# Performance work log

Measured on AMD Instinct MI355X. Metric: run time of the kernel, lower is better.

## Reference

```python
import jax, jax.numpy as jnp
import numpy as np

# config (matches init_kwargs)
WZ, WH, WW = 2, 6, 12            # window_size
Z, H, W = 8, 96, 120             # input_shape after patch embedding
DIM, HEADS = 192, 6
DH = DIM // HEADS
SCALE = DH ** 0.5
NZ, NH, NW = Z // WZ, H // WH, W // WW
NWIN = NZ * NH * NW              # 640 windows (B=1)
TW = NZ * NH                     # type_of_windows = 64
ZHW = WZ * WH * WW               # 144 tokens per window
TABLE = (2 * WW - 1) * WH ** 2 * WZ ** 2  # 3312 bias rows


def _pos_index():
    """Earth-specific relative position index, identical to _construct_index."""
    zi = np.arange(WZ); zj = -np.arange(WZ) * WZ
    hi = np.arange(WH); hj = -np.arange(WH) * WH
    w = np.arange(WW)
    c1 = np.stack(np.meshgrid(zi, hi, w, indexing='ij')).reshape(3, -1)
    c2 = np.stack(np.meshgrid(zj, hj, w, indexing='ij')).reshape(3, -1)
    c = (c1[:, :, None] - c2[:, None, :]).transpose(1, 2, 0)  # (N, N, 3)
    c[..., 2] += WW - 1
    c[..., 1] *= 2 * WW - 1
    c[..., 0] *= (2 * WW - 1) * WH ** 2
    return jnp.asarray(c.sum(-1).reshape(-1), dtype=jnp.int32)  # (ZHW*ZHW,)


def setup_inputs() -> dict:
    key = jax.random.key(0)
    ks = jax.random.split(key, 6)
    x = jax.random.normal(ks[0], (NWIN, ZHW, DIM), jnp.float32)
    # shifted-window style additive mask: 0 or -100
    mask = jnp.where(jax.random.uniform(ks[1], (NWIN, ZHW, ZHW)) < 0.1,
                     jnp.float32(-100.0), jnp.float32(0.0))
    w1 = jax.random.normal(ks[2], (DIM, 3 * DIM), jnp.float32) * 0.02
    b1 = jnp.zeros((3 * DIM,), jnp.float32)
    w2 = jax.random.normal(ks[3], (DIM, DIM), jnp.float32) * 0.02
    b2 = jnp.zeros((DIM,), jnp.float32)
    bias_table = jax.random.normal(ks[4], (TABLE, TW, HEADS), jnp.float32) * 0.02
    pos_index = _pos_index()
    return {"x": x, "mask": mask, "w1": w1, "b1": b1, "w2": w2, "b2": b2,
            "bias_table": bias_table, "pos_index": pos_index}


def reference(x, mask, w1, b1, w2, b2, bias_table, pos_index):
    Bnw, zhw, dim = x.shape
    # qkv projection: (Bnw, zhw, 3*dim) -> (3, Bnw, heads, zhw, dh)
    qkv = (x @ w1 + b1).reshape(Bnw, zhw, 3, HEADS, DH).transpose(2, 0, 3, 1, 4)
    q, k, v = qkv[0], qkv[1], qkv[2]
    attn = jnp.einsum('bhqd,bhkd->bhqk', q, k) / SCALE  # (Bnw, h, zhw, zhw)
    # gather earth-specific bias: (zhw*zhw, TW, h) -> (TW, h, zhw, zhw)
    bias = bias_table[pos_index].reshape(zhw, zhw, TW, HEADS).transpose(2, 3, 0, 1)
    bias = jnp.tile(bias, (Bnw // TW, 1, 1, 1))            # (Bnw, h, zhw, zhw)
    attn = attn + bias
    # additive window mask; broadcast exactly as torch: mask[None, :, None]
    m = jnp.tile(mask, (Bnw // mask.shape[0], 1, 1))
    attn = attn + m[None, :, None]                          # (1, Bnw, h, zhw, zhw)
    attn = jax.nn.softmax(attn, axis=-1)
    out = jnp.matmul(attn, v)                               # (1, Bnw, h, zhw, dh)
    out = jnp.swapaxes(out, 1, 2).reshape(x.shape)          # faithful to torch .transpose(1,2).reshape
    return out @ w2 + b2
```

## Files before the change

kernel.cpp:

```cpp
#include <hip/hip_runtime.h>

#define NWIN 640
#define ZHW  144
#define DIM  192
#define HEADS 6
#define DH   32
#define TW   64
#define C_FOLD 0.25503450f
#define LOG2E 1.4426950408889634f

typedef float f32x4 __attribute__((ext_vector_type(4)));
typedef __bf16 bf16x8 __attribute__((ext_vector_type(8)));

__device__ __forceinline__ unsigned short f2b(float f) {
  unsigned u = __float_as_uint(f);
  u += 0x7fffu + ((u >> 16) & 1u);
  return (unsigned short)(u >> 16);
}
__device__ __forceinline__ unsigned short cvtb(float f) {
  return __builtin_bit_cast(unsigned short, (__bf16)f);
}
__device__ __forceinline__ uint2 pack4(f32x4 a) {
  uint2 r;
  r.x = (unsigned)cvtb(a[0]) | ((unsigned)cvtb(a[1]) << 16);
  r.y = (unsigned)cvtb(a[2]) | ((unsigned)cvtb(a[3]) << 16);
  return r;
}

__device__ __forceinline__ bf16x8 ld_frag(const unsigned short* p) {
  uint2 lo = *(const uint2*)(p);
  uint2 hi = *(const uint2*)(p + 16);
  uint4 u; u.x = lo.x; u.y = lo.y; u.z = hi.x; u.w = hi.y;
  return __builtin_bit_cast(bf16x8, u);
}
#define MFMA16(a, b, c) __builtin_amdgcn_mfma_f32_16x16x32_bf16((a), (b), (c), 0, 0, 0)

#define MP_BIAS0 1440
#define MP_MASK0 2088
#define MP_W0    2728
__global__ __launch_bounds__(256) void megaprep(
    const float* __restrict__ x, const float* __restrict__ mask,
    const float* __restrict__ w1, const float* __restrict__ w2,
    const float* __restrict__ table, const int* __restrict__ pidx,
    unsigned short* __restrict__ xb2, unsigned long long* __restrict__ mq,
    uint4* __restrict__ w1t, uint4* __restrict__ w2t,
    uint2* __restrict__ biasz)
{
  __shared__ __align__(16) unsigned char smem[25088];
  const int tid = threadIdx.x;
  const int b = blockIdx.x;

  if (b < MP_BIAS0) {
    unsigned short (*xl)[196] = (unsigned short(*)[196])smem;
    const int r0 = b * 64;
    const float4* src = (const float4*)(x + (size_t)r0 * DIM);
    float4 v[12];
    #pragma unroll
    for (int u = 0; u < 12; ++u) v[u] = src[tid + 256 * u];
    #pragma unroll
    for (int u = 0; u < 12; ++u) {
      int i = tid + 256 * u;
      int e = i * 4, r = e / DIM, c = e % DIM;
      uint2 pk;
      pk.x = (unsigned)f2b(v[u].x) | ((unsigned)f2b(v[u].y) << 16);
      pk.y = (unsigned)f2b(v[u].z) | ((unsigned)f2b(v[u].w) << 16);
      *(uint2*)(&xl[r][c]) = pk;
    }
    __syncthreads();
    uint4* dst = (uint4*)xb2 + (size_t)b * 1536;
    #pragma unroll
    for (int u = 0; u < 6; ++u) {
      int o = tid + 256 * u;
      int rt = o / 384, rem = o - rt * 384, kk = rem >> 6, ln = rem & 63;
      const unsigned short* p = &xl[16 * rt + (ln & 15)][32 * kk + 4 * (ln >> 4)];
      uint2 lo = *(const uint2*)p;
      uint2 hi = *(const uint2*)(p + 16);
      uint4 u4; u4.x = lo.x; u4.y = lo.y; u4.z = hi.x; u4.w = hi.y;
      dst[o] = u4;
    }
  } else if (b < MP_MASK0) {
    unsigned short (*tile)[49] = (unsigned short(*)[49])smem;
    const int b2 = b - MP_BIAS0;
    const int whc = b2 & 7, rem2 = b2 >> 3;
    const int s = rem2 / 9, kst = rem2 - 9 * (rem2 / 9);
    int rowi[12];
    #pragma unroll
    for (int u = 0; u < 12; ++u) {
      int idx = tid + 256 * u;
      int pos = idx / 12, t = idx - pos * 12;
      int q = 16 * s + (pos >> 4), kk = 16 * kst + (pos & 15);
      (void)t;
      rowi[u] = pidx[q * ZHW + kk];
    }
    float4 v[12];
    #pragma unroll
    for (int u = 0; u < 12; ++u) {
      int idx = tid + 256 * u;
      int pos = idx / 12, t = idx - pos * 12;
      (void)pos;
      v[u] = *(const float4*)(table + (size_t)rowi[u] * 384 + whc * 48 + t * 4);
    }
    #pragma unroll
    for (int u = 0; u < 12; ++u) {
      int idx = tid + 256 * u;
      int pos = idx / 12, t = idx - pos * 12;
      tile[pos][t * 4 + 0] = f2b(v[u].x * LOG2E);
      tile[pos][t * 4 + 1] = f2b(v[u].y * LOG2E);
      tile[pos][t * 4 + 2] = f2b(v[u].z * LOG2E);
      tile[pos][t * 4 + 3] = f2b(v[u].w * LOG2E);
    }
    __syncthreads();
    #pragma unroll
    for (int u = 0; u < 12; ++u) {
      int o = tid + 256 * u;
      int wh = o >> 6, lane = o & 63;
      int lp = (lane & 15) * 16 + 4 * (lane >> 4);
      uint2 uu;
      uu.x = (unsigned)tile[lp + 0][wh] | ((unsigned)tile[lp + 1][wh] << 16);
      uu.y = (unsigned)tile[lp + 2][wh] | ((unsigned)tile[lp + 3][wh] << 16);
      biasz[(((size_t)(whc * 48 + wh) * 9 + s) * 9 + kst) * 64 + lane] = uu;
    }
  } else if (b < MP_W0) {
    unsigned char* ms = (unsigned char*)smem;
    const int win = b - MP_MASK0;
    const float4* src = (const float4*)(mask + (size_t)win * (ZHW * ZHW));
    float4 a[10], c[10];
    #pragma unroll
    for (int u = 0; u < 10; ++u) {
      int i = tid + 256 * u;
      a[u] = src[2 * i];
      c[u] = src[2 * i + 1];
    }
    float4 at, ct;
    if (tid < 32) { at = src[2 * (2560 + tid)]; ct = src[2 * (2560 + tid) + 1]; }
    #pragma unroll
    for (int u = 0; u < 10; ++u) {
      int i = tid + 256 * u;
      unsigned v = (a[u].x == 0.f ? 1u : 0u) | (a[u].y == 0.f ? 2u : 0u) |
                   (a[u].z == 0.f ? 4u : 0u) | (a[u].w == 0.f ? 8u : 0u) |
                   (c[u].x == 0.f ? 16u : 0u) | (c[u].y == 0.f ? 32u : 0u) |
                   (c[u].z == 0.f ? 64u : 0u) | (c[u].w == 0.f ? 128u : 0u);
      ms[i] = (unsigned char)v;
    }
    if (tid < 32) {
      unsigned v = (at.x == 0.f ? 1u : 0u) | (at.y == 0.f ? 2u : 0u) |
                   (at.z == 0.f ? 4u : 0u) | (at.w == 0.f ? 8u : 0u) |
                   (ct.x == 0.f ? 16u : 0u) | (ct.y == 0.f ? 32u : 0u) |
                   (ct.z == 0.f ? 64u : 0u) | (ct.w == 0.f ? 128u : 0u);
      ms[2560 + tid] = (unsigned char)v;
    }
    __syncthreads();
    #pragma unroll
    for (int u = 0; u < 3; ++u) {
      int o = tid + 256 * u;
      if (o < 576) {
        int s = o >> 6, ln = o & 63;
        int qq = 16 * s + (ln & 15), g = ln >> 4;
        int base = qq * 18 + (g >> 1);
        int nsh = 4 * (g & 1);
        unsigned long long mw = 0;
        #pragma unroll
        for (int kst = 0; kst < 9; ++kst) {
          unsigned nib = ((unsigned)ms[base + 2 * kst] >> nsh) & 0xFu;
          mw |= (unsigned long long)nib << (4 * kst);
        }
        mq[(size_t)win * 576 + o] = mw;
      }
    }
  } else {
    int t = (b - MP_W0) * 256 + tid;
    if (t < 13824) {
      int lane = t & 63, r = t >> 6;
      int kk = r % 6, ntg = r / 6;
      int n = ntg * 16 + (lane & 15);
      int k0 = kk * 32 + 4 * ((lane >> 4) & 3);
      float sc = (n < 192) ? C_FOLD : 1.0f;
      unsigned short e[8];
      #pragma unroll
      for (int j = 0; j < 4; ++j) e[j]     = f2b(w1[(size_t)(k0 + j) * 576 + n] * sc);
      #pragma unroll
      for (int j = 0; j < 4; ++j) e[4 + j] = f2b(w1[(size_t)(k0 + 16 + j) * 576 + n] * sc);
      uint4 u;
      u.x = (unsigned)e[0] | ((unsigned)e[1] << 16);
      u.y = (unsigned)e[2] | ((unsigned)e[3] << 16);
      u.z = (unsigned)e[4] | ((unsigned)e[5] << 16);
      u.w = (unsigned)e[6] | ((unsigned)e[7] << 16);
      w1t[t] = u;
    }
    if (t < 4608) {
      int lane = t & 63, r = t >> 6;
      int kk = r % 6, ntg = r / 6;
      int n = ntg * 16 + (lane & 15);
      int k0 = kk * 32 + 4 * ((lane >> 4) & 3);
      unsigned short e[8];
      #pragma unroll
      for (int j = 0; j < 4; ++j) e[j]     = f2b(w2[(size_t)(k0 + j) * 192 + n]);
      #pragma unroll
      for (int j = 0; j < 4; ++j) e[4 + j] = f2b(w2[(size_t)(k0 + 16 + j) * 192 + n]);
      uint4 u;
      u.x = (unsigned)e[0] | ((unsigned)e[1] << 16);
      u.y = (unsigned)e[2] | ((unsigned)e[3] << 16);
      u.z = (unsigned)e[4] | ((unsigned)e[5] << 16);
      u.w = (unsigned)e[6] | ((unsigned)e[7] << 16);
      w2t[t] = u;
    }
  }
}

__global__ __launch_bounds__(256) void qkv_kernel(
    const unsigned short* __restrict__ xb2, const float* __restrict__ b1,
    const uint4* __restrict__ w1t, unsigned short* __restrict__ qkvb)
{
  __shared__ __align__(16) uint4 wb4[2304];
  __shared__ __align__(16) unsigned short bn[4][2][16][38];
  const int tid = threadIdx.x, wv = tid >> 6, lane = tid & 63;
  const int l15 = lane & 15, g = lane >> 4;
  const int b = blockIdx.x;
  const int lid = (b & 7) * 540 + (b >> 3);
  const int mt = lid / 6, ch = lid - mt * 6;
  const int r0 = mt * 128;

  {
    const uint4* wsrc = w1t + (size_t)ch * 2304;
    #pragma unroll 1
    for (int i = tid; i < 2304; i += 256) wb4[i] = wsrc[i];
  }
  bf16x8 xa[2][6];
  {
    const uint4* asrc = (const uint4*)xb2;
    const int rt0 = mt * 8 + 2 * wv;
    #pragma unroll
    for (int rt = 0; rt < 2; ++rt)
      #pragma unroll
      for (int kk = 0; kk < 6; ++kk)
        xa[rt][kk] = __builtin_bit_cast(bf16x8,
            asrc[((size_t)(rt0 + rt) * 6 + kk) * 64 + lane]);
  }
  __syncthreads();
  const int mat = ch >> 1;
  const float bscale = (mat == 0) ? C_FOLD : 1.0f;
  #pragma unroll 1
  for (int hh = 0; hh < 3; ++hh) {
    const int h = (ch & 1) * 3 + hh;
    f32x4 acc[2][2];
    {
      float bv0 = b1[ch * 96 + hh * 32 + l15] * bscale;
      float bv1 = b1[ch * 96 + hh * 32 + 16 + l15] * bscale;
      #pragma unroll
      for (int rt = 0; rt < 2; ++rt) {
        acc[rt][0][0] = bv0; acc[rt][0][1] = bv0; acc[rt][0][2] = bv0; acc[rt][0][3] = bv0;
        acc[rt][1][0] = bv1; acc[rt][1][1] = bv1; acc[rt][1][2] = bv1; acc[rt][1][3] = bv1;
      }
    }
    #pragma unroll
    for (int kk = 0; kk < 6; ++kk) {
      bf16x8 b0  = __builtin_bit_cast(bf16x8, wb4[((2 * hh)     * 6 + kk) * 64 + lane]);
      bf16x8 b1f = __builtin_bit_cast(bf16x8, wb4[((2 * hh + 1) * 6 + kk) * 64 + lane]);
      acc[0][0] = MFMA16(xa[0][kk], b0, acc[0][0]);
      acc[0][1] = MFMA16(xa[0][kk], b1f, acc[0][1]);
      acc[1][0] = MFMA16(xa[1][kk], b0, acc[1][0]);
      acc[1][1] = MFMA16(xa[1][kk], b1f, acc[1][1]);
    }
    if (mat < 2) {
      #pragma unroll
      for (int rt = 0; rt < 2; ++rt)
        #pragma unroll
        for (int ct = 0; ct < 2; ++ct)
          #pragma unroll
          for (int j = 0; j < 4; ++j)
            bn[wv][rt][4 * g + j][16 * ct + l15] = cvtb(acc[rt][ct][j]);
      __builtin_amdgcn_s_waitcnt(0xC07F);
      #pragma unroll
      for (int rt = 0; rt < 2; ++rt) {
        const int row16 = r0 + 32 * wv + 16 * rt;
        const int win = row16 / 144, rg = (row16 - win * 144) >> 4;
        uint2 lo = *(const uint2*)(&bn[wv][rt][l15][4 * g]);
        uint2 hi = *(const uint2*)(&bn[wv][rt][l15][16 + 4 * g]);
        uint4 u; u.x = lo.x; u.y = lo.y; u.z = hi.x; u.w = hi.y;
        ((uint4*)qkvb)[((size_t)((mat * HEADS + h) * NWIN + win)) * 576 + rg * 64 + lane] = u;
      }
      __builtin_amdgcn_s_waitcnt(0xC07F);
    } else {
      #pragma unroll
      for (int rt = 0; rt < 2; ++rt) {
        const int row16 = r0 + 32 * wv + 16 * rt;
        const int win = row16 / 144, rg = (row16 - win * 144) >> 4;
        uint2* dst = (uint2*)qkvb + ((size_t)((mat * HEADS + h) * NWIN + win)) * 1152
                     + (rg * 2) * 64 + lane;
        #pragma unroll
        for (int ct = 0; ct < 2; ++ct) dst[ct * 64] = pack4(acc[rt][ct]);
      }
    }
  }
}

#define VT_LD 164
__global__ __launch_bounds__(576, 4) void attn6_kernel(
    const uint4* __restrict__ qf, const uint4* __restrict__ kf,
    const uint2* __restrict__ vf, const uint2* __restrict__ biasz,
    const unsigned long long* __restrict__ mq, unsigned short* __restrict__ xbuf)
{
  __shared__ __align__(16) uint4 ks[2][576];
  __shared__ __align__(16) unsigned short vt[2][DH][VT_LD];
  const int tid = threadIdx.x, wv = tid >> 6, lane = tid & 63;
  const int l15 = lane & 15, g = lane >> 4;
  const int b = blockIdx.x, win = b >> 1, hg = b & 1, h0 = 3 * hg;
  const int wtype = win & (TW - 1);
  const int s = wv;
  const int q = 16 * s + l15;
  const int m0 = h0 * NWIN + win;

  const unsigned long long mw = mq[((size_t)win * 9 + s) * 64 + lane];

  {
    ks[0][tid] = kf[(size_t)m0 * 576 + tid];
    const uint2* vs = vf + (size_t)m0 * 1152;
    #pragma unroll
    for (int t = 0; t < 2; ++t) {
      int i = tid + t * 576;
      int fid = i >> 6, ln = i & 63;
      int tok = 16 * (fid >> 1) + 4 * (ln >> 4);
      int d = 16 * (fid & 1) + (ln & 15);
      *(uint2*)(&vt[0][d][tok]) = vs[i];
    }
    #pragma unroll 1
    for (int i = tid; i < 2 * DH * 10; i += 576) {
      int buf = i / 320, rem = i - buf * 320;
      int r = rem / 10, c = 144 + (rem - r * 10) * 2;
      *(unsigned*)(&vt[buf][r][c]) = 0;
    }
  }
  __syncthreads();

  #pragma unroll 1
  for (int hh = 0; hh < 3; ++hh) {
    const int cur = hh & 1;
    const int h = h0 + hh;
    const int m = m0 + hh * NWIN;
    uint2 bb[9];
    {
      const uint2* bz = biasz + (((size_t)(wtype * HEADS + h) * 9 + s) * 9) * 64 + lane;
      #pragma unroll
      for (int kst = 0; kst < 9; ++kst) bb[kst] = bz[kst * 64];
    }
    const bf16x8 bq = __builtin_bit_cast(bf16x8, qf[(size_t)m * 576 + s * 64 + lane]);
    uint4 kreg;
    uint2 vr0, vr1;
    if (hh < 2) {
      kreg = kf[(size_t)(m + NWIN) * 576 + tid];
      const uint2* vs = vf + (size_t)(m + NWIN) * 1152;
      vr0 = vs[tid];
      vr1 = vs[tid + 576];
    }
    float sum = 0.f;
    uint4 pb[5];
    uint2 lo_pk;
    #pragma unroll
    for (int kst = 0; kst < 9; ++kst) {
      f32x4 c;
      c[0] = __uint_as_float(bb[kst].x << 16);
      c[1] = __uint_as_float(bb[kst].x & 0xffff0000u);
      c[2] = __uint_as_float(bb[kst].y << 16);
      c[3] = __uint_as_float(bb[kst].y & 0xffff0000u);
      f32x4 sv = MFMA16(__builtin_bit_cast(bf16x8, ks[cur][kst * 64 + lane]), bq, c);
      const unsigned nib = (unsigned)(mw >> (4 * kst)) & 0xFu;
      #pragma unroll
      for (int j = 0; j < 4; ++j) {
        float p = __builtin_amdgcn_exp2f(sv[j]);
        int keep = ((int)(nib << (31 - j))) >> 31;
        p = __uint_as_float(__float_as_uint(p) & (unsigned)keep);
        sv[j] = p;
        sum += p;
      }
      uint2 pk = pack4(sv);
      if (kst & 1) {
        pb[kst >> 1].x = lo_pk.x; pb[kst >> 1].y = lo_pk.y;
        pb[kst >> 1].z = pk.x;    pb[kst >> 1].w = pk.y;
      } else {
        lo_pk = pk;
      }
    }
    pb[4].x = lo_pk.x; pb[4].y = lo_pk.y; pb[4].z = 0; pb[4].w = 0;
    sum += __shfl_xor(sum, 16);
    sum += __shfl_xor(sum, 32);
    const float inv = 1.f / sum;
    const int r = q / 6, cb = (q - r * 6) * DH;
    unsigned short* xrow = xbuf + (size_t)(24 * m + r) * DIM + cb + 4 * g;
    #pragma unroll
    for (int dt = 0; dt < 2; ++dt) {
      const unsigned short* vrow = &vt[cur][dt * 16 + l15][4 * g];
      f32x4 ot; ot[0] = 0.f; ot[1] = 0.f; ot[2] = 0.f; ot[3] = 0.f;
      #pragma unroll
      for (int s5 = 0; s5 < 5; ++s5)
        ot = MFMA16(ld_frag(vrow + s5 * 32), __builtin_bit_cast(bf16x8, pb[s5]), ot);
      ot[0] *= inv; ot[1] *= inv; ot[2] *= inv; ot[3] *= inv;
      *(uint2*)(xrow + dt * 16) = pack4(ot);
    }
    if (hh < 2) {
      ks[cur ^ 1][tid] = kreg;
      #pragma unroll
      for (int t = 0; t < 2; ++t) {
        int i = tid + t * 576;
        int fid = i >> 6, ln = i & 63;
        int tok = 16 * (fid >> 1) + 4 * (ln >> 4);
        int d = 16 * (fid & 1) + (ln & 15);
        *(uint2*)(&vt[cur ^ 1][d][tok]) = (t == 0) ? vr0 : vr1;
      }
    }
    __syncthreads();
  }
}

__global__ __launch_bounds__(512) void proj_kernel(
    const unsigned short* __restrict__ xbuf, const uint4* __restrict__ w2t,
    const float* __restrict__ b2, float* __restrict__ out)
{
  __shared__ __align__(16) uint4 wb4[2304];
  const int tid = threadIdx.x, wv = tid >> 6, lane = tid & 63;
  const int l15 = lane & 15, g = lane >> 4;
  const int r0 = blockIdx.x * 128;
  bf16x8 xa[6];
  {
    const unsigned short* xrow = xbuf + (size_t)(r0 + 16 * wv + l15) * DIM;
    #pragma unroll
    for (int kk = 0; kk < 6; ++kk) xa[kk] = ld_frag(xrow + kk * 32 + 4 * g);
  }
  #pragma unroll 1
  for (int ch = 0; ch < 2; ++ch) {
    __syncthreads();
    {
      const uint4* wsrc = w2t + (size_t)ch * 2304;
      #pragma unroll 1
      for (int i = tid; i < 2304; i += 512) wb4[i] = wsrc[i];
    }
    __syncthreads();
    #pragma unroll 1
    for (int nt = 0; nt < 6; ++nt) {
      const int n = ch * 96 + nt * 16 + l15;
      float bv = b2[n];
      f32x4 acc; acc[0] = bv; acc[1] = bv; acc[2] = bv; acc[3] = bv;
      #pragma unroll
      for (int kk = 0; kk < 6; ++kk)
        acc = MFMA16(xa[kk], __builtin_bit_cast(bf16x8, wb4[(nt * 6 + kk) * 64 + lane]), acc);
      #pragma unroll
      for (int j = 0; j < 4; ++j)
        out[(size_t)(r0 + 16 * wv + 4 * g + j) * DIM + n] = acc[j];
    }
  }
}

extern "C" void kernel_launch(void* const* d_in, const int* in_sizes, int n_in,
                              void* d_out, int out_size, void* d_ws, size_t ws_size,
                              hipStream_t stream)
{
  const float* x     = (const float*)d_in[0];
  const float* mask  = (const float*)d_in[1];
  const float* w1    = (const float*)d_in[2];
  const float* b1    = (const float*)d_in[3];
  const float* w2    = (const float*)d_in[4];
  const float* b2    = (const float*)d_in[5];
  const float* table = (const float*)d_in[6];
  const int*   pidx  = (const int*)d_in[7];
  float* out = (float*)d_out;
  unsigned char* ws = (unsigned char*)d_ws;
  uint4* w1t            = (uint4*)(ws);
  uint4* w2t            = (uint4*)(ws + 221184);
  uint2* biasz          = (uint2*)(ws + 294912);
  unsigned long long* mq = (unsigned long long*)(ws + 16220160);
  unsigned short* qkvb  = (unsigned short*)(ws + 29491200);
  unsigned short* xbuf  = (unsigned short*)(ws + 135659520);
  unsigned short* xb2   = xbuf;

  const uint4* qf = (const uint4*)qkvb;
  const uint4* kf = (const uint4*)(ws + 29491200 + 35389440);
  const uint2* vf = (const uint2*)(ws + 29491200 + 70778880);

  megaprep  <<<dim3(2782), dim3(256), 0, stream>>>(x, mask, w1, w2, table, pidx,
                                                   xb2, mq, w1t, w2t, biasz);
  qkv_kernel<<<dim3(4320), dim3(256), 0, stream>>>(xb2, b1, w1t, qkvb);
  attn6_kernel<<<dim3(1280), dim3(576), 0, stream>>>(qf, kf, vf, biasz, mq, xbuf);
  proj_kernel<<<dim3(720), dim3(512), 0, stream>>>(xbuf, w2t, b2, out);
}
```

Before: 139.6 us.

## Fuse output projection into attention kernel, eliminating the intermediate bf16 buffer

The attention kernel now keeps each head's output in registers, stages the three heads' 72x192 output rows in shared memory (reusing the K/V buffers), and applies the W2 projection plus bias directly before writing fp32 results. This removes the separate proj_kernel launch and the global round trip through xbuf. In exchange each block reads W2 fragments straight from global/L2 rather than staging them in LDS, and the projection work is split unevenly across 9 waves (60 tiles, the last partly padded).

```diff
diff --git a/kernel.cpp b/kernel.cpp
--- a/kernel.cpp
+++ b/kernel.cpp
@@ -87,9 +87,8 @@
     #pragma unroll
     for (int u = 0; u < 12; ++u) {
       int idx = tid + 256 * u;
-      int pos = idx / 12, t = idx - pos * 12;
+      int pos = idx / 12;
       int q = 16 * s + (pos >> 4), kk = 16 * kst + (pos & 15);
-      (void)t;
       rowi[u] = pidx[q * ZHW + kk];
     }
     float4 v[12];
@@ -97,7 +96,6 @@
     for (int u = 0; u < 12; ++u) {
       int idx = tid + 256 * u;
       int pos = idx / 12, t = idx - pos * 12;
-      (void)pos;
       v[u] = *(const float4*)(table + (size_t)rowi[u] * 384 + whc * 48 + t * 4);
     }
     #pragma unroll
@@ -295,13 +293,18 @@
 }
 
 #define VT_LD 164
-__global__ __launch_bounds__(576, 4) void attn6_kernel(
+#define OL_LD 200
+__global__ __launch_bounds__(576, 4) void attn7_kernel(
     const uint4* __restrict__ qf, const uint4* __restrict__ kf,
     const uint2* __restrict__ vf, const uint2* __restrict__ biasz,
-    const unsigned long long* __restrict__ mq, unsigned short* __restrict__ xbuf)
+    const unsigned long long* __restrict__ mq, const uint4* __restrict__ w2t,
+    const float* __restrict__ b2, float* __restrict__ out)
 {
-  __shared__ __align__(16) uint4 ks[2][576];
-  __shared__ __align__(16) unsigned short vt[2][DH][VT_LD];
+  __shared__ __align__(16) unsigned char smem[39424];
+  uint4 (*ks)[576] = (uint4(*)[576])smem;
+  unsigned short (*vt)[DH][VT_LD] =
+      (unsigned short(*)[DH][VT_LD])(smem + 18432);
+  unsigned short (*ol)[OL_LD] = (unsigned short(*)[OL_LD])smem;
   const int tid = threadIdx.x, wv = tid >> 6, lane = tid & 63;
   const int l15 = lane & 15, g = lane >> 4;
   const int b = blockIdx.x, win = b >> 1, hg = b & 1, h0 = 3 * hg;
@@ -332,6 +335,7 @@
   }
   __syncthreads();
 
+  uint2 oreg[3][2];
   #pragma unroll 1
   for (int hh = 0; hh < 3; ++hh) {
     const int cur = hh & 1;
@@ -384,8 +388,6 @@
     sum += __shfl_xor(sum, 16);
     sum += __shfl_xor(sum, 32);
     const float inv = 1.f / sum;
-    const int r = q / 6, cb = (q - r * 6) * DH;
-    unsigned short* xrow = xbuf + (size_t)(24 * m + r) * DIM + cb + 4 * g;
     #pragma unroll
     for (int dt = 0; dt < 2; ++dt) {
       const unsigned short* vrow = &vt[cur][dt * 16 + l15][4 * g];
@@ -394,7 +396,7 @@
       for (int s5 = 0; s5 < 5; ++s5)
         ot = MFMA16(ld_frag(vrow + s5 * 32), __builtin_bit_cast(bf16x8, pb[s5]), ot);
       ot[0] *= inv; ot[1] *= inv; ot[2] *= inv; ot[3] *= inv;
-      *(uint2*)(xrow + dt * 16) = pack4(ot);
+      oreg[hh][dt] = pack4(ot);
     }
     if (hh < 2) {
       ks[cur ^ 1][tid] = kreg;
@@ -409,42 +411,34 @@
     }
     __syncthreads();
   }
-}
-
-__global__ __launch_bounds__(512) void proj_kernel(
-    const unsigned short* __restrict__ xbuf, const uint4* __restrict__ w2t,
-    const float* __restrict__ b2, float* __restrict__ out)
-{
-  __shared__ __align__(16) uint4 wb4[2304];
-  const int tid = threadIdx.x, wv = tid >> 6, lane = tid & 63;
-  const int l15 = lane & 15, g = lane >> 4;
-  const int r0 = blockIdx.x * 128;
-  bf16x8 xa[6];
+
   {
-    const unsigned short* xrow = xbuf + (size_t)(r0 + 16 * wv + l15) * DIM;
-    #pragma unroll
-    for (int kk = 0; kk < 6; ++kk) xa[kk] = ld_frag(xrow + kk * 32 + 4 * g);
-  }
+    const int r = q / 6, cb = (q - r * 6) * DH;
+    #pragma unroll
+    for (int hh = 0; hh < 3; ++hh) {
+      *(uint2*)(&ol[hh * 24 + r][cb + 4 * g]) = oreg[hh][0];
+      *(uint2*)(&ol[hh * 24 + r][cb + 16 + 4 * g]) = oreg[hh][1];
+    }
+  }
+  __syncthreads();
   #pragma unroll 1
-  for (int ch = 0; ch < 2; ++ch) {
-    __syncthreads();
-    {
-      const uint4* wsrc = w2t + (size_t)ch * 2304;
-      #pragma unroll 1
-      for (int i = tid; i < 2304; i += 512) wb4[i] = wsrc[i];
-    }
-    __syncthreads();
-    #pragma unroll 1
-    for (int nt = 0; nt < 6; ++nt) {
-      const int n = ch * 96 + nt * 16 + l15;
-      float bv = b2[n];
-      f32x4 acc; acc[0] = bv; acc[1] = bv; acc[2] = bv; acc[3] = bv;
-      #pragma unroll
-      for (int kk = 0; kk < 6; ++kk)
-        acc = MFMA16(xa[kk], __builtin_bit_cast(bf16x8, wb4[(nt * 6 + kk) * 64 + lane]), acc);
-      #pragma unroll
-      for (int j = 0; j < 4; ++j)
-        out[(size_t)(r0 + 16 * wv + 4 * g + j) * DIM + n] = acc[j];
+  for (int p = wv; p < 60; p += 9) {
+    const int rt2 = p / 12, nt = p - rt2 * 12;
+    float bv = b2[nt * 16 + l15];
+    f32x4 acc; acc[0] = bv; acc[1] = bv; acc[2] = bv; acc[3] = bv;
+    const unsigned short* arow = &ol[16 * rt2 + l15][4 * g];
+    #pragma unroll
+    for (int kk = 0; kk < 6; ++kk)
+      acc = MFMA16(ld_frag(arow + kk * 32),
+                   __builtin_bit_cast(bf16x8, w2t[(nt * 6 + kk) * 64 + lane]), acc);
+    #pragma unroll
+    for (int j = 0; j < 4; ++j) {
+      int rr = 16 * rt2 + 4 * g + j;
+      if (rr < 72) {
+        int hh2 = rr / 24, r2 = rr - hh2 * 24;
+        size_t grow = (size_t)(24 * ((h0 + hh2) * NWIN + win) + r2);
+        out[grow * DIM + nt * 16 + l15] = acc[j];
+      }
     }
   }
 }
@@ -468,8 +462,7 @@
   uint2* biasz          = (uint2*)(ws + 294912);
   unsigned long long* mq = (unsigned long long*)(ws + 16220160);
   unsigned short* qkvb  = (unsigned short*)(ws + 29491200);
-  unsigned short* xbuf  = (unsigned short*)(ws + 135659520);
-  unsigned short* xb2   = xbuf;
+  unsigned short* xb2   = (unsigned short*)(ws + 135659520);
 
   const uint4* qf = (const uint4*)qkvb;
   const uint4* kf = (const uint4*)(ws + 29491200 + 35389440);
@@ -478,6 +471,6 @@
   megaprep  <<<dim3(2782), dim3(256), 0, stream>>>(x, mask, w1, w2, table, pidx,
                                                    xb2, mq, w1t, w2t, biasz);
   qkv_kernel<<<dim3(4320), dim3(256), 0, stream>>>(xb2, b1, w1t, qkvb);
-  attn6_kernel<<<dim3(1280), dim3(576), 0, stream>>>(qf, kf, vf, biasz, mq, xbuf);
-  proj_kernel<<<dim3(720), dim3(512), 0, stream>>>(xbuf, w2t, b2, out);
-}
+  attn7_kernel<<<dim3(1280), dim3(576), 0, stream>>>(qf, kf, vf, biasz, mq,
+                                                     w2t, b2, out);
+}
```

Result: slower. 152.4 us (+9.1%).
